# Kernel tuning notes

Measured on AMD Instinct MI355X. Metric: run time of the kernel, lower is better.

## Reference

```python
import jax, jax.numpy as jnp
import numpy as np

D = 256      # d_model
SUB = 3      # number of adjacency subsets
GROUPS = 8
N, T, V = 32, 256, 19


def setup_inputs() -> dict:
    key = jax.random.key(0)
    ks = jax.random.split(key, 4)
    return {
        "x": jax.random.normal(ks[0], (N, T, V, D), jnp.float32),
        "para": jax.random.normal(ks[1], (3, GROUPS, V, V), jnp.float32),
        "linear_weight": jax.random.normal(ks[2], (D, D * SUB), jnp.float32) * 0.05,
        "linear_bias": jax.random.normal(ks[3], (1, D * SUB, 1, 1), jnp.float32) * 0.05,
        "bn_gamma": jnp.ones((D * SUB,), jnp.float32),
        "bn_beta": jnp.zeros((D * SUB,), jnp.float32),
        "bn1_gamma": jnp.ones((D,), jnp.float32),
        "bn1_beta": jnp.zeros((D,), jnp.float32),
    }


def _bn(x, gamma, beta, eps=1e-5):
    # BatchNorm2d (training mode): stats over (n, t, v) per channel
    m = jnp.mean(x, axis=(0, 2, 3), keepdims=True)
    v = jnp.var(x, axis=(0, 2, 3), keepdims=True)
    return (x - m) * jax.lax.rsqrt(v + eps) * gamma[None, :, None, None] + beta[None, :, None, None]


def reference(x, para, linear_weight, linear_bias, bn_gamma, bn_beta, bn1_gamma, bn1_beta):
    xc = jnp.transpose(x, (0, 3, 1, 2))                 # (n, c, t, v)
    # expand per-group adjacency to per-channel: (3, D, V, V)
    A = jnp.tile(para, (1, D // GROUPS, 1, 1))
    # L2 row-normalize along last dim (matches torch.norm(dim=-1))
    A = A / (jnp.linalg.norm(A, axis=-1, keepdims=True) + 1e-4)
    # channel mixing: (n, 3c, t, v)
    y = jnp.einsum('nctw,cd->ndtw', xc, linear_weight)
    y = _bn(y + linear_bias, bn_gamma, bn_beta)
    n, kc, t, v = y.shape
    y = y.reshape(n, SUB, kc // SUB, t, v)              # (n, k, c, t, v)
    # per-channel tiny 19x19 adjacency matmul
    y = jnp.einsum('nkctv,kcvw->nctw', y, A)            # (n, c, t, v)
    out = jax.nn.relu(_bn(y + xc, bn1_gamma, bn1_beta))
    return jnp.transpose(out, (0, 2, 3, 1))             # (n, t, v, c)
```

## Files before the change

### kernel.cpp

```cpp
#include <hip/hip_runtime.h>

typedef unsigned short u16;
typedef unsigned int u32;
typedef float f32x4 __attribute__((ext_vector_type(4)));
typedef __bf16 bf16x8 __attribute__((ext_vector_type(8)));

#define M_ALL 155648.0f
#define GP 168

__device__ __forceinline__ u16 f2bf(float f) {
  union { float f; u32 u; } x; x.f = f;
  u32 u = x.u;
  u += 0x7FFFu + ((u >> 16) & 1u);
  return (u16)(u >> 16);
}
__device__ __forceinline__ float bf2f(u16 h) {
  union { u32 u; float f; } x; x.u = ((u32)h) << 16;
  return x.f;
}
__device__ __forceinline__ f32x4 zero4() { f32x4 z = {0.f, 0.f, 0.f, 0.f}; return z; }

__device__ __forceinline__ int xs_idx(int m, int c) {
  return m * 256 + ((((c >> 3) ^ (m & 7)) << 3) | (c & 7));
}
__device__ __forceinline__ int y2_idx(int r, int kvp) {
  int sw = (r & 7) ^ ((r >> 3) & 7);
  return r * 64 + ((((kvp >> 3) ^ sw) << 3) | (kvp & 7));
}

__global__ void k_prep(const float* __restrict__ para, u16* __restrict__ wa2) {
  __shared__ float aL[3 * 8 * 19 * 19];
  int tid = threadIdx.x;
  if (tid < 456) {
    int k = tid / 152, rem = tid % 152, g = rem / 19, v = rem % 19;
    int base = ((k * 8 + g) * 19 + v) * 19;
    float ss = 0.f;
    #pragma unroll
    for (int w = 0; w < 19; ++w) { float a = para[base + w]; ss += a * a; }
    float inv = 1.f / (sqrtf(ss) + 1e-4f);
    #pragma unroll
    for (int w = 0; w < 19; ++w) aL[base + w] = para[base + w] * inv;
  }
  __syncthreads();
  for (int i = tid; i < 8 * 20 * 64; i += 512) {
    int g = i / 1280, rem = i % 1280, w = rem >> 6, kvp = rem & 63;
    u16 val = 0;
    if (w < 19 && kvp < 57) {
      int k = kvp / 19, v = kvp - 19 * k;
      val = f2bf(aL[((k * 8 + g) * 19 + v) * 19 + w]);
    }
    wa2[i] = val;
  }
}

__global__ void k_wt(const float* __restrict__ W, u16* __restrict__ wt) {
  int idx = blockIdx.x * 512 + threadIdx.x;
  int d = idx >> 8, c = idx & 255;
  wt[idx] = f2bf(W[c * 768 + d]);
}

__global__ __launch_bounds__(512, 2) void k_gram(const float* __restrict__ x,
                                                 float* __restrict__ Gp,
                                                 float* __restrict__ colsum) {
  __shared__ u16 xsT[256 * GP];
  __shared__ float scs[512];
  int tid = threadIdx.x, bid = blockIdx.x;
  int c = tid & 255, mh = tid >> 8;
  int lane = tid & 63, wave = tid >> 6;
  int cl = lane & 15, q = lane >> 4;

  if (tid < 256) {
    *reinterpret_cast<uint2*>(&xsT[tid * GP + 152]) = make_uint2(0u, 0u);
    *reinterpret_cast<uint2*>(&xsT[tid * GP + 156]) = make_uint2(0u, 0u);
  }

  float cs = 0.f;
  f32x4 acc[2][16];
  #pragma unroll
  for (int ri = 0; ri < 2; ++ri)
    #pragma unroll
    for (int j = 0; j < 16; ++j) acc[ri][j] = zero4();

  for (int ss = 0; ss < 4; ++ss) {
    int sl = bid * 4 + ss;
    const float* xb = x + (size_t)sl * 152 * 256;
    __syncthreads();
    #pragma unroll 1
    for (int it = 0; it < 19; ++it) {
      int m0 = it * 8 + mh * 4;
      float v0 = xb[(m0 + 0) * 256 + c];
      float v1 = xb[(m0 + 1) * 256 + c];
      float v2 = xb[(m0 + 2) * 256 + c];
      float v3 = xb[(m0 + 3) * 256 + c];
      cs += v0 + v1 + v2 + v3;
      uint2 p;
      p.x = (u32)f2bf(v0) | ((u32)f2bf(v1) << 16);
      p.y = (u32)f2bf(v2) | ((u32)f2bf(v3) << 16);
      *reinterpret_cast<uint2*>(&xsT[c * GP + m0]) = p;
    }
    __syncthreads();
    #pragma unroll
    for (int s = 0; s < 5; ++s) {
      int kof = s * 32 + q * 8;
      bf16x8 a0 = *reinterpret_cast<const bf16x8*>(&xsT[(wave * 16 + cl) * GP + kof]);
      bf16x8 a1 = *reinterpret_cast<const bf16x8*>(&xsT[((wave + 8) * 16 + cl) * GP + kof]);
      #pragma unroll
      for (int ct2 = 0; ct2 < 16; ++ct2) {
        bf16x8 b = *reinterpret_cast<const bf16x8*>(&xsT[(ct2 * 16 + cl) * GP + kof]);
        acc[0][ct2] = __builtin_amdgcn_mfma_f32_16x16x32_bf16(a0, b, acc[0][ct2], 0, 0, 0);
        acc[1][ct2] = __builtin_amdgcn_mfma_f32_16x16x32_bf16(a1, b, acc[1][ct2], 0, 0, 0);
      }
    }
  }
  #pragma unroll
  for (int ri = 0; ri < 2; ++ri) {
    int ct = wave + ri * 8;
    int tb = 16 * ct - (ct * (ct - 1)) / 2 - ct;
    #pragma unroll
    for (int ct2 = 0; ct2 < 16; ++ct2) {
      if (ct2 >= ct) {
        float* dst = Gp + ((size_t)(tb + ct2) * 256 + bid) * 256;
        #pragma unroll
        for (int r4 = 0; r4 < 4; ++r4)
          dst[(q * 4 + r4) * 16 + cl] = acc[ri][ct2][r4];
      }
    }
  }
  scs[tid] = cs;
  __syncthreads();
  if (tid < 256) atomicAdd(&colsum[tid], scs[tid] + scs[tid + 256]);
}

__global__ __launch_bounds__(256) void k_red(const float* __restrict__ Gp,
                                             float* __restrict__ G) {
  int b = blockIdx.x;
  int e = threadIdx.x;
  int ct = 0;
  #pragma unroll
  for (int t = 1; t < 16; ++t)
    if (b >= 16 * t - (t * (t - 1)) / 2) ct = t;
  int ct2 = ct + (b - (16 * ct - (ct * (ct - 1)) / 2));
  const float* src = Gp + (size_t)b * 65536;
  float s = 0.f;
  #pragma unroll 8
  for (int p = 0; p < 256; ++p) s += src[p * 256 + e];
  int row = e >> 4, col = e & 15;
  int rr = ct * 16 + row, cc = ct2 * 16 + col;
  G[rr * 256 + cc] = s;
  G[cc * 256 + rr] = s;
}

__global__ __launch_bounds__(256) void k_f1(const float* __restrict__ G,
                                            const float* __restrict__ colsum,
                                            const float* __restrict__ W,
                                            const float* __restrict__ gam,
                                            const float* __restrict__ bet,
                                            float* __restrict__ ST) {
  __shared__ float wd[256];
  __shared__ float red[16];
  int d = blockIdx.x, c = threadIdx.x;
  float wv = W[c * 768 + d];
  wd[c] = wv;
  __syncthreads();
  float dot = 0.f;
  const float* Gr = G + c * 256;
  #pragma unroll 4
  for (int j = 0; j < 256; ++j) dot += Gr[j] * wd[j];
  float part = wv * dot;
  float mpart = colsum[c] * wv;
  #pragma unroll
  for (int o = 32; o; o >>= 1) { part += __shfl_down(part, o); mpart += __shfl_down(mpart, o); }
  int lane = c & 63, w = c >> 6;
  if (lane == 0) { red[w] = part; red[8 + w] = mpart; }
  __syncthreads();
  if (c == 0) {
    float qv = red[0] + red[1] + red[2] + red[3];
    float ms = red[8] + red[9] + red[10] + red[11];
    float mean = ms / M_ALL;
    float var = qv / M_ALL - mean * mean;
    float S = gam[d] * rsqrtf(var + 1e-5f);
    ST[d] = S;
    ST[768 + d] = bet[d] - mean * S;
  }
}

__global__ __launch_bounds__(512, 2) void k_main(const float* __restrict__ x,
                                                 const u16* __restrict__ wt,
                                                 const u16* __restrict__ wa2,
                                                 const float* __restrict__ ST,
                                                 float* __restrict__ sumz,
                                                 float* __restrict__ out) {
  __shared__ u16 xs[152 * 256];
  __shared__ u16 y2[512 * 64];
  __shared__ float scrz[1024];
  int tid = threadIdx.x;
  int bid = blockIdx.x;
  const float* xbase = x + (size_t)bid * 152 * 256;
  size_t obase = (size_t)bid * 152 * 256;

  {
    int r = tid >> 6, c4 = (tid & 63) << 2;
    for (int it = 0; it < 19; ++it) {
      int m = it * 8 + r;
      float4 f = *reinterpret_cast<const float4*>(xbase + m * 256 + c4);
      uint2 p;
      p.x = (u32)f2bf(f.x) | ((u32)f2bf(f.y) << 16);
      p.y = (u32)f2bf(f.z) | ((u32)f2bf(f.w) << 16);
      *reinterpret_cast<uint2*>(&xs[xs_idx(m, c4)]) = p;
    }
  }

  int lane = tid & 63, wave = tid >> 6;
  int mhalf = wave & 1, nt3 = wave >> 1;
  int cl = lane & 15, q = lane >> 4;
  int g = wave;
  const bf16x8* wtv = reinterpret_cast<const bf16x8*>(wt);
  float* zbufF = reinterpret_cast<float*>(y2);

  bf16x8 bfr[2][2];
  #pragma unroll
  for (int ks = 0; ks < 2; ++ks)
    #pragma unroll
    for (int nt = 0; nt < 2; ++nt) {
      int w = nt * 16 + cl; int wc = (w < 20) ? w : 19;
      bfr[ks][nt] = *reinterpret_cast<const bf16x8*>(&wa2[(g * 20 + wc) * 64 + ks * 32 + q * 8]);
    }

  int arow[5], mlow[5];
  #pragma unroll
  for (int i = 0; i < 5; ++i) {
    int rr = mhalf * 80 + i * 16 + cl;
    if (rr > 151) rr = 151;
    arow[i] = rr * 256; mlow[i] = rr & 7;
  }
  __syncthreads();

  for (int nc = 0; nc < 4; ++nc) {
    f32x4 acc[5][3];
    #pragma unroll
    for (int i = 0; i < 5; ++i)
      #pragma unroll
      for (int jj = 0; jj < 3; ++jj) acc[i][jj] = zero4();
    for (int s = 0; s < 8; ++s) {
      int sq4 = s * 4 + q;
      bf16x8 b[3];
      #pragma unroll
      for (int jj = 0; jj < 3; ++jj) {
        int j = nt3 * 3 + jj;
        int d = (j >> 2) * 256 + nc * 64 + (j & 3) * 16 + cl;
        b[jj] = wtv[d * 32 + sq4];
      }
      #pragma unroll
      for (int i = 0; i < 5; ++i) {
        bf16x8 a = *reinterpret_cast<const bf16x8*>(&xs[arow[i] + ((sq4 ^ mlow[i]) << 3)]);
        #pragma unroll
        for (int jj = 0; jj < 3; ++jj)
          acc[i][jj] = __builtin_amdgcn_mfma_f32_16x16x32_bf16(a, b[jj], acc[i][jj], 0, 0, 0);
      }
    }
    __syncthreads();

    #pragma unroll
    for (int kk = 0; kk < 7; ++kk)
      y2[y2_idx(tid, 57 + kk)] = 0;

    #pragma unroll
    for (int jj = 0; jj < 3; ++jj) {
      int j = nt3 * 3 + jj;
      int ksub = j >> 2;
      int c_local = (j & 3) * 16 + cl;
      int d = ksub * 256 + nc * 64 + c_local;
      float Sc = ST[d], Tc = ST[768 + d];
      #pragma unroll
      for (int i = 0; i < 5; ++i) {
        int mb = mhalf * 80 + i * 16 + q * 4;
        #pragma unroll
        for (int r4 = 0; r4 < 4; ++r4) {
          int m = mb + r4;
          if (m < 152) {
            int t = (m * 27) >> 9;
            int v = m - t * 19;
            int kvp = ksub * 19 + v;
            int r = t * 64 + c_local;
            y2[y2_idx(r, kvp)] = f2bf(acc[i][jj][r4] * Sc + Tc);
          }
        }
      }
    }
    __syncthreads();

    f32x4 zacc[4][2];
    #pragma unroll
    for (int mt = 0; mt < 4; ++mt) { zacc[mt][0] = zero4(); zacc[mt][1] = zero4(); }
    #pragma unroll
    for (int ks = 0; ks < 2; ++ks) {
      #pragma unroll
      for (int mt = 0; mt < 4; ++mt) {
        int tc = mt * 16 + cl;
        int t = tc >> 3, c8 = tc & 7;
        int r = t * 64 + c8 * 8 + g;
        int ch = (ks * 4 + q) ^ g ^ c8;
        bf16x8 afr = *reinterpret_cast<const bf16x8*>(&y2[r * 64 + (ch << 3)]);
        #pragma unroll
        for (int nt = 0; nt < 2; ++nt)
          zacc[mt][nt] = __builtin_amdgcn_mfma_f32_16x16x32_bf16(afr, bfr[ks][nt], zacc[mt][nt], 0, 0, 0);
      }
    }
    __syncthreads();

    #pragma unroll
    for (int mt = 0; mt < 4; ++mt)
      #pragma unroll
      for (int nt = 0; nt < 2; ++nt) {
        int w = nt * 16 + cl;
        if (w < 19) {
          #pragma unroll
          for (int r4 = 0; r4 < 4; ++r4) {
            int mm = mt * 16 + q * 4 + r4;
            int t = mm >> 3, c8 = mm & 7;
            zbufF[(c8 * 8 + g) * 153 + t * 19 + w] = zacc[mt][nt][r4];
          }
        }
      }
    __syncthreads();

    float sz = 0.f, sq = 0.f;
    int cloc = tid & 63;
    int cglob = nc * 64 + cloc;
    #pragma unroll 1
    for (int rep = 0; rep < 19; ++rep) {
      int mp = rep * 8 + (tid >> 6);
      float z = zbufF[cloc * 153 + mp] + bf2f(xs[xs_idx(mp, cglob)]);
      out[obase + (size_t)mp * 256 + cglob] = z;
      sz += z; sq += z * z;
    }
    scrz[(tid >> 6) * 64 + cloc] = sz;
    scrz[512 + (tid >> 6) * 64 + cloc] = sq;
    __syncthreads();
    if (tid < 128) {
      int comp = tid >> 6, c = tid & 63;
      float v = 0.f;
      #pragma unroll
      for (int h = 0; h < 8; ++h) v += scrz[comp * 512 + h * 64 + c];
      atomicAdd(&sumz[comp * 256 + nc * 64 + c], v);
    }
  }
}

__global__ void k_f2(const float* __restrict__ statz, const float* __restrict__ gam,
                     const float* __restrict__ bet, float* __restrict__ S1T1) {
  int c = threadIdx.x;
  float inv = 1.f / M_ALL;
  float mz = statz[c] * inv;
  float qv = statz[256 + c] * inv;
  float var = qv - mz * mz;
  float Sc = gam[c] * rsqrtf(var + 1e-5f);
  S1T1[c] = Sc;
  S1T1[256 + c] = bet[c] - mz * Sc;
}

__global__ __launch_bounds__(256) void k_relu(float* __restrict__ out,
                                              const float* __restrict__ S1T1) {
  int tid = threadIdx.x;
  int lane = tid & 63;
  int wv = ((blockIdx.x << 8) + tid) >> 6;
  const float4* s14 = reinterpret_cast<const float4*>(S1T1);
  float4 sv = s14[lane], tv = s14[64 + lane];
  float4* o4 = reinterpret_cast<float4*>(out);
  #pragma unroll 1
  for (int r = 0; r < 19; ++r) {
    size_t i = ((size_t)r * 8192 + wv) * 64 + lane;
    float4 f = o4[i];
    f.x = fmaxf(f.x * sv.x + tv.x, 0.f);
    f.y = fmaxf(f.y * sv.y + tv.y, 0.f);
    f.z = fmaxf(f.z * sv.z + tv.z, 0.f);
    f.w = fmaxf(f.w * sv.w + tv.w, 0.f);
    o4[i] = f;
  }
}

extern "C" void kernel_launch(void* const* d_in, const int* in_sizes, int n_in,
                              void* d_out, int out_size, void* d_ws, size_t ws_size,
                              hipStream_t stream) {
  const float* x    = (const float*)d_in[0];
  const float* para = (const float*)d_in[1];
  const float* W    = (const float*)d_in[2];
  const float* bng  = (const float*)d_in[4];
  const float* bnb  = (const float*)d_in[5];
  const float* bn1g = (const float*)d_in[6];
  const float* bn1b = (const float*)d_in[7];
  float* out = (float*)d_out;

  char* ws = (char*)d_ws;
  u16* wt     = (u16*)ws;
  u16* wa2    = (u16*)(ws + 393216);
  float* G    = (float*)(ws + 413696);
  float* csum = (float*)(ws + 675840);
  float* sumz = (float*)(ws + 676864);
  float* ST   = (float*)(ws + 678912);
  float* S1T1 = (float*)(ws + 685056);
  float* Gp   = (float*)(ws + 687104);

  hipMemsetAsync(ws + 675840, 0, 1024 + 2048, stream);
  k_prep<<<dim3(1),    dim3(512), 0, stream>>>(para, wa2);
  k_wt  <<<dim3(384),  dim3(512), 0, stream>>>(W, wt);
  k_gram<<<dim3(256),  dim3(512), 0, stream>>>(x, Gp, csum);
  k_red <<<dim3(136),  dim3(256), 0, stream>>>(Gp, G);
  k_f1  <<<dim3(768),  dim3(256), 0, stream>>>(G, csum, W, bng, bnb, ST);
  k_main<<<dim3(1024), dim3(512), 0, stream>>>(x, wt, wa2, ST, sumz, out);
  k_f2  <<<dim3(1),    dim3(256), 0, stream>>>(sumz, bn1g, bn1b, S1T1);
  k_relu<<<dim3(2048), dim3(256), 0, stream>>>(out, S1T1);
}
```

Baseline: 608.2 us.

## Pre-convert x to bf16 once and reuse it in Gram and main kernels

Adds a conversion kernel that writes a bf16 copy of x into workspace and computes the per-channel column sums. The Gram and main kernels then read half-width bf16 data instead of converting fp32 themselves. The Gp partial buffer moves into the output buffer to free workspace space. This adds an extra pass that writes about 80MB, in exchange for cutting the fp32 reads in the two heavy kernels. The new path only runs when the workspace is large enough, otherwise the old path is used.

```diff
diff --git a/kernel.cpp b/kernel.cpp
--- a/kernel.cpp
+++ b/kernel.cpp
@@ -59,7 +59,39 @@
   wt[idx] = f2bf(W[c * 768 + d]);
 }
 
+__global__ __launch_bounds__(512) void k_cvt(const float* __restrict__ x,
+                                             u16* __restrict__ xbf,
+                                             float* __restrict__ colsum) {
+  __shared__ float scs[2048];
+  int tid = threadIdx.x;
+  float p0 = 0.f, p1 = 0.f, p2 = 0.f, p3 = 0.f;
+  const float4* x4 = reinterpret_cast<const float4*>(x);
+  ushort4* o4 = reinterpret_cast<ushort4*>(xbf);
+  #pragma unroll 1
+  for (size_t idx = (size_t)blockIdx.x * 512 + tid; idx < 9961472u; idx += 524288u) {
+    float4 f = x4[idx];
+    ushort4 o;
+    o.x = f2bf(f.x); o.y = f2bf(f.y); o.z = f2bf(f.z); o.w = f2bf(f.w);
+    o4[idx] = o;
+    p0 += f.x; p1 += f.y; p2 += f.z; p3 += f.w;
+  }
+  int c4 = tid & 63, w8 = tid >> 6;
+  scs[w8 * 256 + c4 * 4 + 0] = p0;
+  scs[w8 * 256 + c4 * 4 + 1] = p1;
+  scs[w8 * 256 + c4 * 4 + 2] = p2;
+  scs[w8 * 256 + c4 * 4 + 3] = p3;
+  __syncthreads();
+  if (tid < 256) {
+    float s = 0.f;
+    #pragma unroll
+    for (int h = 0; h < 8; ++h) s += scs[h * 256 + tid];
+    atomicAdd(&colsum[tid], s);
+  }
+}
+
+template<int BF>
 __global__ __launch_bounds__(512, 2) void k_gram(const float* __restrict__ x,
+                                                 const u16* __restrict__ xbf,
                                                  float* __restrict__ Gp,
                                                  float* __restrict__ colsum) {
   __shared__ u16 xsT[256 * GP];
@@ -83,20 +115,36 @@
 
   for (int ss = 0; ss < 4; ++ss) {
     int sl = bid * 4 + ss;
-    const float* xb = x + (size_t)sl * 152 * 256;
-    __syncthreads();
-    #pragma unroll 1
-    for (int it = 0; it < 19; ++it) {
-      int m0 = it * 8 + mh * 4;
-      float v0 = xb[(m0 + 0) * 256 + c];
-      float v1 = xb[(m0 + 1) * 256 + c];
-      float v2 = xb[(m0 + 2) * 256 + c];
-      float v3 = xb[(m0 + 3) * 256 + c];
-      cs += v0 + v1 + v2 + v3;
-      uint2 p;
-      p.x = (u32)f2bf(v0) | ((u32)f2bf(v1) << 16);
-      p.y = (u32)f2bf(v2) | ((u32)f2bf(v3) << 16);
-      *reinterpret_cast<uint2*>(&xsT[c * GP + m0]) = p;
+    __syncthreads();
+    if constexpr (BF) {
+      const u16* xb16 = xbf + (size_t)sl * 152 * 256;
+      #pragma unroll 4
+      for (int it = 0; it < 19; ++it) {
+        int m0 = it * 8 + mh * 4;
+        u32 v0 = xb16[(m0 + 0) * 256 + c];
+        u32 v1 = xb16[(m0 + 1) * 256 + c];
+        u32 v2 = xb16[(m0 + 2) * 256 + c];
+        u32 v3 = xb16[(m0 + 3) * 256 + c];
+        uint2 p;
+        p.x = v0 | (v1 << 16);
+        p.y = v2 | (v3 << 16);
+        *reinterpret_cast<uint2*>(&xsT[c * GP + m0]) = p;
+      }
+    } else {
+      const float* xb = x + (size_t)sl * 152 * 256;
+      #pragma unroll 1
+      for (int it = 0; it < 19; ++it) {
+        int m0 = it * 8 + mh * 4;
+        float v0 = xb[(m0 + 0) * 256 + c];
+        float v1 = xb[(m0 + 1) * 256 + c];
+        float v2 = xb[(m0 + 2) * 256 + c];
+        float v3 = xb[(m0 + 3) * 256 + c];
+        cs += v0 + v1 + v2 + v3;
+        uint2 p;
+        p.x = (u32)f2bf(v0) | ((u32)f2bf(v1) << 16);
+        p.y = (u32)f2bf(v2) | ((u32)f2bf(v3) << 16);
+        *reinterpret_cast<uint2*>(&xsT[c * GP + m0]) = p;
+      }
     }
     __syncthreads();
     #pragma unroll
@@ -126,9 +174,11 @@
       }
     }
   }
-  scs[tid] = cs;
-  __syncthreads();
-  if (tid < 256) atomicAdd(&colsum[tid], scs[tid] + scs[tid + 256]);
+  if constexpr (!BF) {
+    scs[tid] = cs;
+    __syncthreads();
+    if (tid < 256) atomicAdd(&colsum[tid], scs[tid] + scs[tid + 256]);
+  }
 }
 
 __global__ __launch_bounds__(256) void k_red(const float* __restrict__ Gp,
@@ -184,7 +234,9 @@
   }
 }
 
+template<int BF>
 __global__ __launch_bounds__(512, 2) void k_main(const float* __restrict__ x,
+                                                 const u16* __restrict__ xbf,
                                                  const u16* __restrict__ wt,
                                                  const u16* __restrict__ wa2,
                                                  const float* __restrict__ ST,
@@ -195,10 +247,22 @@
   __shared__ float scrz[1024];
   int tid = threadIdx.x;
   int bid = blockIdx.x;
-  const float* xbase = x + (size_t)bid * 152 * 256;
   size_t obase = (size_t)bid * 152 * 256;
 
-  {
+  if constexpr (BF) {
+    const u16* xb16 = xbf + (size_t)bid * 152 * 256;
+    int w = tid >> 6, lane = tid & 63;
+    int ch = lane & 31, half = lane >> 5;
+    for (int it = 0; it < 10; ++it) {
+      int m = it * 16 + 2 * w + half;
+      if (m < 152) {
+        const u16* src = xb16 + m * 256 + ((ch ^ (m & 7)) << 3);
+        *reinterpret_cast<bf16x8*>(&xs[m * 256 + (ch << 3)]) =
+            *reinterpret_cast<const bf16x8*>(src);
+      }
+    }
+  } else {
+    const float* xbase = x + (size_t)bid * 152 * 256;
     int r = tid >> 6, c4 = (tid & 63) << 2;
     for (int it = 0; it < 19; ++it) {
       int m = it * 8 + r;
@@ -399,15 +463,26 @@
   float* sumz = (float*)(ws + 676864);
   float* ST   = (float*)(ws + 678912);
   float* S1T1 = (float*)(ws + 685056);
-  float* Gp   = (float*)(ws + 687104);
+  u16* xbf    = (u16*)(ws + 687104);
+  float* Gp   = (float*)d_out;
+
+  const size_t NEED = 687104u + 79691776u;
 
   hipMemsetAsync(ws + 675840, 0, 1024 + 2048, stream);
   k_prep<<<dim3(1),    dim3(512), 0, stream>>>(para, wa2);
   k_wt  <<<dim3(384),  dim3(512), 0, stream>>>(W, wt);
-  k_gram<<<dim3(256),  dim3(512), 0, stream>>>(x, Gp, csum);
-  k_red <<<dim3(136),  dim3(256), 0, stream>>>(Gp, G);
-  k_f1  <<<dim3(768),  dim3(256), 0, stream>>>(G, csum, W, bng, bnb, ST);
-  k_main<<<dim3(1024), dim3(512), 0, stream>>>(x, wt, wa2, ST, sumz, out);
+  if (ws_size >= NEED) {
+    k_cvt <<<dim3(1024), dim3(512), 0, stream>>>(x, xbf, csum);
+    k_gram<1><<<dim3(256),  dim3(512), 0, stream>>>(x, xbf, Gp, csum);
+    k_red <<<dim3(136),  dim3(256), 0, stream>>>(Gp, G);
+    k_f1  <<<dim3(768),  dim3(256), 0, stream>>>(G, csum, W, bng, bnb, ST);
+    k_main<1><<<dim3(1024), dim3(512), 0, stream>>>(x, xbf, wt, wa2, ST, sumz, out);
+  } else {
+    k_gram<0><<<dim3(256),  dim3(512), 0, stream>>>(x, nullptr, Gp, csum);
+    k_red <<<dim3(136),  dim3(256), 0, stream>>>(Gp, G);
+    k_f1  <<<dim3(768),  dim3(256), 0, stream>>>(G, csum, W, bng, bnb, ST);
+    k_main<0><<<dim3(1024), dim3(512), 0, stream>>>(x, nullptr, wt, wa2, ST, sumz, out);
+  }
   k_f2  <<<dim3(1),    dim3(256), 0, stream>>>(sumz, bn1g, bn1b, S1T1);
   k_relu<<<dim3(2048), dim3(256), 0, stream>>>(out, S1T1);
 }
```

Result: no change. 613.9 us (+0.9%).
